# Performance work log

Hardware: AMD Instinct MI355X
Metric: run time of the kernel (lower is better)

## Reference

```python
import jax, jax.numpy as jnp
import numpy as np

B, S, D = 4, 2048, 1024

def _xavier(key, shape):
    bound = float(np.sqrt(6.0 / (shape[0] + shape[1])))
    return jax.random.uniform(key, shape, dtype=jnp.float32, minval=-bound, maxval=bound)

def setup_inputs() -> dict:
    key = jax.random.key(0)
    k0, k1, k2, k3 = jax.random.split(key, 4)
    return {
        "embeddings": jax.random.normal(k0, (B, S, D), dtype=jnp.float32),
        "W_Q": _xavier(k1, (D, D)),
        "W_K": _xavier(k2, (D, D)),
        "W_V": _xavier(k3, (D, D)),
    }

def reference(embeddings, W_Q, W_K, W_V):
    _, seq_len, d = embeddings.shape
    Q = embeddings @ W_Q                      # [B,S,D]
    K = embeddings @ W_K
    V = embeddings @ W_V
    scale = 1.0 / jnp.sqrt(jnp.float32(d))
    scores = jnp.einsum('bqd,bkd->bqk', Q, K) * scale   # [B,S,S]
    causal = jnp.tril(jnp.ones((seq_len, seq_len), dtype=bool))
    scores = jnp.where(causal[None, :, :], scores, -jnp.inf)
    probs = jax.nn.softmax(scores, axis=-1)
    return jnp.einsum('bqk,bkd->bqd', probs, V)
```

## Files before the change

kernel.cpp:

```cpp
#include <hip/hip_runtime.h>
#include <hip/hip_bf16.h>

#define BSZ 4
#define SEQ 2048
#define DIM 1024

typedef __attribute__((ext_vector_type(8))) short bf16x8;
typedef __attribute__((ext_vector_type(4))) float floatx4;

__device__ __forceinline__ unsigned short f2bf(float x) {
  union { float f; unsigned int u; } v; v.f = x;
  unsigned int r = v.u + 0x7fffu + ((v.u >> 16) & 1u);
  return (unsigned short)(r >> 16);
}

template <typename T> __device__ __forceinline__ void store_c(T* p, float v);
template <> __device__ __forceinline__ void store_c<float>(float* p, float v) { *p = v; }
template <> __device__ __forceinline__ void store_c<unsigned short>(unsigned short* p, float v) { *p = f2bf(v); }

__global__ __launch_bounds__(256) void prep(const float* __restrict__ E,
                                            const float* __restrict__ Wq,
                                            const float* __restrict__ Wk,
                                            const float* __restrict__ Wv,
                                            unsigned short* __restrict__ Ebf,
                                            unsigned short* __restrict__ Wqbf,
                                            unsigned short* __restrict__ Wkbf,
                                            unsigned short* __restrict__ WtV,
                                            float* __restrict__ rsum) {
  __shared__ float tile[32][33];
  int b = blockIdx.x;
  int tid = threadIdx.x;
  if (b < 10240) {
    const float* src;
    unsigned short* dst;
    int base;
    if (b < 8192) {
      if (b < 8) {
        int j = b * 1024 + tid * 4;
        *(float4*)(rsum + j) = make_float4(0.f, 0.f, 0.f, 0.f);
      }
      src = E; dst = Ebf; base = b;
    } else if (b < 9216) {
      src = Wq; dst = Wqbf; base = b - 8192;
    } else {
      src = Wk; dst = Wkbf; base = b - 9216;
    }
    int i = (base * 256 + tid) * 4;
    float4 v = *(const float4*)(src + i);
    ushort4 o;
    o.x = f2bf(v.x); o.y = f2bf(v.y); o.z = f2bf(v.z); o.w = f2bf(v.w);
    *(ushort4*)(dst + i) = o;
  } else {
    int rb = b - 10240;
    int bx = rb & 31, by = rb >> 5;
    int n0 = bx * 32, k0 = by * 32;
    int tx = tid & 31, ty = tid >> 5;
    for (int r = ty; r < 32; r += 8)
      tile[r][tx] = Wv[(size_t)(k0 + r) * DIM + n0 + tx];
    __syncthreads();
    for (int r = ty; r < 32; r += 8)
      WtV[(size_t)(n0 + r) * DIM + k0 + tx] = f2bf(tile[tx][r]);
  }
}

__device__ __forceinline__ void gload16(const unsigned short* g, unsigned short* l) {
  __builtin_amdgcn_global_load_lds(
      (const __attribute__((address_space(1))) unsigned int*)g,
      (__attribute__((address_space(3))) unsigned int*)l, 16, 0, 0);
}

#define NT_PROJ 32

template <int BMt>
__device__ __forceinline__ void proj_core(
    const unsigned short* __restrict__ A,
    const unsigned short* __restrict__ Bm,
    unsigned short* __restrict__ C, int ldc, int m0, int n0,
    unsigned short* sAr, unsigned short* sBr) {
  constexpr int LPA = BMt / 128;
  constexpr int LPT = LPA + 2;
  constexpr int FR  = BMt / 32;
  constexpr int TA  = BMt * 32;
  constexpr int TB  = 256 * 32;

  const int tid = threadIdx.x;
  const int lane = tid & 63;
  const int wid = tid >> 6;
  const int wm = (wid >> 2) * (BMt / 2);
  const int wn = (wid & 3) * 64;
  const int lr = lane & 15, lq = lane >> 4;

  const int srow = tid >> 2;
  const int schunk = (tid & 3) ^ ((tid >> 3) & 3);
  const unsigned short* gA = A + (size_t)(m0 + srow) * DIM + schunk * 8;
  const unsigned short* gB = Bm + (size_t)(n0 + srow) * DIM + schunk * 8;
  unsigned short* lA = sAr + 16 * 32 * wid;
  unsigned short* lB = sBr + 16 * 32 * wid;
  const size_t swG = (size_t)128 * DIM;

#define STAGE_A(T) do { int rb_ = (T) & 3; \
    gload16(gA + (size_t)(T) * 32, lA + rb_ * TA); \
    if constexpr (LPA == 2) gload16(gA + (size_t)(T) * 32 + swG, lA + rb_ * TA + 4096); } while (0)
#define STAGE_B(T) do { int rb_ = (T) & 3; \
    gload16(gB + (size_t)(T) * 32,       lB + rb_ * TB); \
    gload16(gB + (size_t)(T) * 32 + swG, lB + rb_ * TB + 4096); } while (0)
#define ARD(rb_, rowv) (*(const bf16x8*)&sAr[(rb_) * TA + (rowv) * 32 + (lq ^ (((rowv) >> 1) & 3)) * 8])
#define BRD(rb_, rowv) (*(const bf16x8*)&sBr[(rb_) * TB + (rowv) * 32 + (lq ^ (((rowv) >> 1) & 3)) * 8])

  floatx4 acc[FR][4] = {};

  STAGE_A(0); STAGE_B(0);
  STAGE_A(1); STAGE_B(1);
  STAGE_A(2); STAGE_B(2);
  if constexpr (LPT == 4) asm volatile("s_waitcnt vmcnt(8)" ::: "memory");
  else                    asm volatile("s_waitcnt vmcnt(6)" ::: "memory");
  __builtin_amdgcn_s_barrier();

#pragma unroll 4
  for (int T = 0; T < NT_PROJ; ++T) {
    const int rb = T & 3;
    bf16x8 af[4], bfr[4];
#pragma unroll
    for (int j = 0; j < 4; ++j) bfr[j] = BRD(rb, wn + j * 16 + lr);
#pragma unroll
    for (int i = 0; i < 4; ++i) af[i] = ARD(rb, wm + i * 16 + lr);
    if (T + 3 < NT_PROJ) {
      STAGE_A(T + 3);
      if constexpr (BMt == 128) STAGE_B(T + 3);
    }
    __builtin_amdgcn_s_barrier();
    __builtin_amdgcn_s_setprio(1);
#pragma unroll
    for (int i = 0; i < 4; ++i)
#pragma unroll
      for (int j = 0; j < 4; ++j)
        acc[i][j] = __builtin_amdgcn_mfma_f32_16x16x32_bf16(af[i], bfr[j], acc[i][j], 0, 0, 0);
    __builtin_amdgcn_s_setprio(0);
    if constexpr (BMt == 256) {
      __builtin_amdgcn_s_barrier();
#pragma unroll
      for (int i = 0; i < 4; ++i) af[i] = ARD(rb, wm + 64 + i * 16 + lr);
      if (T + 3 < NT_PROJ) STAGE_B(T + 3);
      __builtin_amdgcn_s_barrier();
      __builtin_amdgcn_s_setprio(1);
#pragma unroll
      for (int i = 0; i < 4; ++i)
#pragma unroll
        for (int j = 0; j < 4; ++j)
          acc[4 + i][j] = __builtin_amdgcn_mfma_f32_16x16x32_bf16(af[i], bfr[j], acc[4 + i][j], 0, 0, 0);
      __builtin_amdgcn_s_setprio(0);
    }
    if (T < NT_PROJ - 3) {
      if constexpr (LPT == 4) asm volatile("s_waitcnt vmcnt(8)" ::: "memory");
      else                    asm volatile("s_waitcnt vmcnt(6)" ::: "memory");
    } else if (T == NT_PROJ - 3) {
      if constexpr (LPT == 4) asm volatile("s_waitcnt vmcnt(4)" ::: "memory");
      else                    asm volatile("s_waitcnt vmcnt(3)" ::: "memory");
    } else if (T == NT_PROJ - 2) {
      asm volatile("s_waitcnt vmcnt(0)" ::: "memory");
    }
    __builtin_amdgcn_s_barrier();
  }
#undef STAGE_A
#undef STAGE_B
#undef ARD
#undef BRD

#pragma unroll
  for (int i = 0; i < FR; ++i) {
    int rbase = m0 + wm + i * 16 + lq * 4;
#pragma unroll
    for (int j = 0; j < 4; ++j) {
      int col = n0 + wn + j * 16 + lr;
#pragma unroll
      for (int r = 0; r < 4; ++r)
        C[(size_t)(rbase + r) * ldc + col] = f2bf(acc[i][j][r]);
    }
  }
}

__global__ __launch_bounds__(512, 2) void bulk1(
    const unsigned short* __restrict__ Wkbf,
    const unsigned short* __restrict__ Wqbf,
    const unsigned short* __restrict__ Ebf,
    const unsigned short* __restrict__ WtV,
    unsigned short* __restrict__ Mt,
    unsigned short* __restrict__ Vt) {
  __shared__ __align__(16) unsigned short sA[16384];
  __shared__ __align__(16) unsigned short sB[32768];
  int x = blockIdx.x;
  if (x < 32) {
    proj_core<128>(Wkbf, Wqbf, Mt, DIM, (x >> 2) * 128, (x & 3) * 256, sA, sB);
  } else {
    x -= 32;
    proj_core<128>(WtV, Ebf, Vt, BSZ * SEQ, (x >> 5) * 128, (x & 31) * 256, sA, sB);
  }
}

__global__ __launch_bounds__(512, 2) void bulk2(
    const unsigned short* __restrict__ Ebf,
    const unsigned short* __restrict__ Mt,
    unsigned short* __restrict__ EM) {
  __shared__ __align__(16) unsigned short sA[16384];
  __shared__ __align__(16) unsigned short sB[32768];
  int x = blockIdx.x;
  proj_core<128>(Ebf, Mt, EM, DIM, (x >> 2) * 128, (x & 3) * 256, sA, sB);
}

template <typename OutT, int MODE>
__global__ __launch_bounds__(256, 2) void gemm_ring(
    const unsigned short* __restrict__ A, int lda, long long strideA,
    const unsigned short* __restrict__ B, int ldb, long long strideB,
    OutT* __restrict__ C, int ldc, long long strideC,
    int Kdim, float scale, float* __restrict__ rowsum) {
  int m0, n0;
  if constexpr (MODE == 1) {
    int t = blockIdx.x;
    int mt = 0;
    while (((mt + 1) * (mt + 2)) / 2 <= t) mt++;
    int nt = t - (mt * (mt + 1)) / 2;
    m0 = mt * 128; n0 = nt * 128;
  } else {
    int yy = ((blockIdx.z >> 1) & 1) ? blockIdx.y : (gridDim.y - 1 - blockIdx.y);
    m0 = yy * 128;
    n0 = blockIdx.x * 128;
  }
  const int Keff = (MODE == 2) ? min(Kdim, m0 + 128) : Kdim;
  const int NT = Keff >> 5;
  A += (long long)blockIdx.z * strideA;
  B += (long long)blockIdx.z * strideB;
  C += (long long)blockIdx.z * strideC;
  rowsum += (size_t)blockIdx.z * SEQ;

  __shared__ __align__(16) unsigned short sA[4 * 4096];
  __shared__ __align__(16) unsigned short sB[4 * 4096];

  const int tid = threadIdx.x;
  const int lane = tid & 63;
  const int wid = tid >> 6;
  const int wm = (wid >> 1) * 64, wn = (wid & 1) * 64;
  const int lr = lane & 15, lq = lane >> 4;

  const int schunk = (tid & 3) ^ ((tid >> 3) & 3);
  const unsigned short* gA = A + (size_t)(m0 + (tid >> 2)) * lda + schunk * 8;
  const unsigned short* gB = B + (size_t)(n0 + (tid >> 2)) * ldb + schunk * 8;
  unsigned short* lA = sA + wid * 512;
  unsigned short* lB = sB + wid * 512;
  const size_t sGA = (size_t)64 * lda, sGB = (size_t)64 * ldb;

#define RSTAGE(T) do { int rb_ = (T) & 3; \
    gload16(gA + (size_t)(T) * 32,       lA + rb_ * 4096); \
    gload16(gA + (size_t)(T) * 32 + sGA, lA + rb_ * 4096 + 2048); \
    gload16(gB + (size_t)(T) * 32,       lB + rb_ * 4096); \
    gload16(gB + (size_t)(T) * 32 + sGB, lB + rb_ * 4096 + 2048); } while (0)
#define RARD(rb_, rowv) (*(const bf16x8*)&sA[(rb_) * 4096 + (rowv) * 32 + (lq ^ (((rowv) >> 1) & 3)) * 8])
#define RBRD(rb_, rowv) (*(const bf16x8*)&sB[(rb_) * 4096 + (rowv) * 32 + (lq ^ (((rowv) >> 1) & 3)) * 8])

  floatx4 acc[4][4] = {};

  RSTAGE(0); RSTAGE(1); RSTAGE(2);
  asm volatile("s_waitcnt vmcnt(8)" ::: "memory");
  __builtin_amdgcn_s_barrier();

  for (int T = 0; T < NT; ++T) {
    const int rb = T & 3;
    bf16x8 af[4], bfr[4];
#pragma unroll
    for (int j = 0; j < 4; ++j) bfr[j] = RBRD(rb, wn + j * 16 + lr);
#pragma unroll
    for (int i = 0; i < 4; ++i) af[i] = RARD(rb, wm + i * 16 + lr);
    if (T + 3 < NT) RSTAGE(T + 3);
    __builtin_amdgcn_s_barrier();
    __builtin_amdgcn_s_setprio(1);
#pragma unroll
    for (int i = 0; i < 4; ++i)
#pragma unroll
      for (int j = 0; j < 4; ++j)
        acc[i][j] = __builtin_amdgcn_mfma_f32_16x16x32_bf16(af[i], bfr[j], acc[i][j], 0, 0, 0);
    __builtin_amdgcn_s_setprio(0);
    if (T < NT - 3)       asm volatile("s_waitcnt vmcnt(8)" ::: "memory");
    else if (T == NT - 3) asm volatile("s_waitcnt vmcnt(4)" ::: "memory");
    else if (T == NT - 2) asm volatile("s_waitcnt vmcnt(0)" ::: "memory");
    __builtin_amdgcn_s_barrier();
  }
#undef RSTAGE
#undef RARD
#undef RBRD

  if constexpr (MODE == 1) {
#pragma unroll
    for (int i = 0; i < 4; i++) {
      int rbase = m0 + wm + i * 16 + lq * 4;
      float s0 = 0.f, s1 = 0.f, s2 = 0.f, s3 = 0.f;
#pragma unroll
      for (int j = 0; j < 4; j++) {
        int col = n0 + wn + j * 16 + lr;
        float e0 = (col <= rbase + 0) ? __expf(acc[i][j][0] * scale) : 0.0f;
        float e1 = (col <= rbase + 1) ? __expf(acc[i][j][1] * scale) : 0.0f;
        float e2 = (col <= rbase + 2) ? __expf(acc[i][j][2] * scale) : 0.0f;
        float e3 = (col <= rbase + 3) ? __expf(acc[i][j][3] * scale) : 0.0f;
        store_c(&C[(size_t)(rbase + 0) * ldc + col], e0);
        store_c(&C[(size_t)(rbase + 1) * ldc + col], e1);
        store_c(&C[(size_t)(rbase + 2) * ldc + col], e2);
        store_c(&C[(size_t)(rbase + 3) * ldc + col], e3);
        s0 += e0; s1 += e1; s2 += e2; s3 += e3;
      }
#pragma unroll
      for (int m = 1; m < 16; m <<= 1) {
        s0 += __shfl_xor(s0, m, 64);
        s1 += __shfl_xor(s1, m, 64);
        s2 += __shfl_xor(s2, m, 64);
        s3 += __shfl_xor(s3, m, 64);
      }
      if (lr == 0) {
        atomicAdd(&rowsum[rbase + 0], s0);
        atomicAdd(&rowsum[rbase + 1], s1);
        atomicAdd(&rowsum[rbase + 2], s2);
        atomicAdd(&rowsum[rbase + 3], s3);
      }
    }
  } else {
#pragma unroll
    for (int i = 0; i < 4; i++) {
      int rbase = m0 + wm + i * 16 + lq * 4;
      float i0 = 1.0f / rowsum[rbase + 0];
      float i1 = 1.0f / rowsum[rbase + 1];
      float i2 = 1.0f / rowsum[rbase + 2];
      float i3 = 1.0f / rowsum[rbase + 3];
#pragma unroll
      for (int j = 0; j < 4; j++) {
        int col = n0 + wn + j * 16 + lr;
        store_c(&C[(size_t)(rbase + 0) * ldc + col], acc[i][j][0] * i0);
        store_c(&C[(size_t)(rbase + 1) * ldc + col], acc[i][j][1] * i1);
        store_c(&C[(size_t)(rbase + 2) * ldc + col], acc[i][j][2] * i2);
        store_c(&C[(size_t)(rbase + 3) * ldc + col], acc[i][j][3] * i3);
      }
    }
  }
}

extern "C" void kernel_launch(void* const* d_in, const int* in_sizes, int n_in,
                              void* d_out, int out_size, void* d_ws, size_t ws_size,
                              hipStream_t stream) {
  const float* E  = (const float*)d_in[0];
  const float* Wq = (const float*)d_in[1];
  const float* Wk = (const float*)d_in[2];
  const float* Wv = (const float*)d_in[3];
  float* out = (float*)d_out;

  char* ws = (char*)d_ws;
  size_t off = 0;
  auto alloc = [&](size_t bytes) {
    void* p = ws + off;
    off += (bytes + 255) & ~(size_t)255;
    return p;
  };
  const size_t M_ALL = (size_t)BSZ * SEQ;
  unsigned short* Ebf  = (unsigned short*)alloc(M_ALL * DIM * 2);
  unsigned short* Wqbf = (unsigned short*)alloc((size_t)DIM * DIM * 2);
  unsigned short* Wkbf = (unsigned short*)alloc((size_t)DIM * DIM * 2);
  unsigned short* WtV  = (unsigned short*)alloc((size_t)DIM * DIM * 2);
  unsigned short* Mt   = (unsigned short*)alloc((size_t)DIM * DIM * 2);
  unsigned short* EM   = (unsigned short*)alloc(M_ALL * DIM * 2);
  unsigned short* Vt   = (unsigned short*)alloc((size_t)DIM * M_ALL * 2);
  unsigned short* ExpS = (unsigned short*)alloc((size_t)BSZ * SEQ * SEQ * 2);
  float*          Rsum = (float*)alloc((size_t)BSZ * SEQ * 4);

  prep<<<dim3(11264), dim3(256), 0, stream>>>(E, Wq, Wk, Wv, Ebf, Wqbf, Wkbf, WtV, Rsum);

  bulk1<<<dim3(288), dim3(512), 0, stream>>>(Wkbf, Wqbf, Ebf, WtV, Mt, Vt);

  bulk2<<<dim3(256), dim3(512), 0, stream>>>(Ebf, Mt, EM);

  gemm_ring<unsigned short, 1><<<dim3(136, 1, BSZ), dim3(256), 0, stream>>>(
      EM, DIM, (long long)SEQ * DIM,
      Ebf, DIM, (long long)SEQ * DIM,
      ExpS, SEQ, (long long)SEQ * SEQ,
      DIM, 0.03125f , Rsum);

  gemm_ring<float, 2><<<dim3(8, 16, BSZ), dim3(256), 0, stream>>>(
      ExpS, SEQ, (long long)SEQ * SEQ,
      Vt, (int)M_ALL, (long long)SEQ,
      out, DIM, (long long)SEQ * DIM,
      SEQ, 1.0f, Rsum);
}
```

Baseline: 241.0 us.

## Compute Wk·Wqᵀ inside prep from fp32 and merge projection kernels

The small Mt = Wk·Wqᵀ GEMM moves into the prep kernel as 64 extra blocks. These blocks load fp32 weights directly, convert them to bf16 in registers and use a register-prefetched LDS MFMA loop. This drops the separate bf16 copies of Wq and Wk and their buffers. With Mt ready after prep, the V projection and the E·Mt projection merge into one launch, removing a kernel boundary and a dependent stage. The cost is that 64 heavy GEMM blocks now run inside a memory-bound conversion kernel and may form a tail.

```diff
diff --git a/kernel.cpp b/kernel.cpp
--- a/kernel.cpp
+++ b/kernel.cpp
@@ -12,6 +12,17 @@
   union { float f; unsigned int u; } v; v.f = x;
   unsigned int r = v.u + 0x7fffu + ((v.u >> 16) & 1u);
   return (unsigned short)(r >> 16);
+}
+
+__device__ __forceinline__ uint4 ld8f(const float* p) {
+  float4 a = *(const float4*)p;
+  float4 b = *(const float4*)(p + 4);
+  uint4 u;
+  u.x = (unsigned)f2bf(a.x) | ((unsigned)f2bf(a.y) << 16);
+  u.y = (unsigned)f2bf(a.z) | ((unsigned)f2bf(a.w) << 16);
+  u.z = (unsigned)f2bf(b.x) | ((unsigned)f2bf(b.y) << 16);
+  u.w = (unsigned)f2bf(b.z) | ((unsigned)f2bf(b.w) << 16);
+  return u;
 }
 
 template <typename T> __device__ __forceinline__ void store_c(T* p, float v);
@@ -23,43 +34,109 @@
                                             const float* __restrict__ Wk,
                                             const float* __restrict__ Wv,
                                             unsigned short* __restrict__ Ebf,
-                                            unsigned short* __restrict__ Wqbf,
-                                            unsigned short* __restrict__ Wkbf,
                                             unsigned short* __restrict__ WtV,
+                                            unsigned short* __restrict__ Mt,
                                             float* __restrict__ rsum) {
-  __shared__ float tile[32][33];
+  __shared__ __align__(16) unsigned short As[128][72];
+  __shared__ __align__(16) unsigned short Bs[128][72];
   int b = blockIdx.x;
   int tid = threadIdx.x;
-  if (b < 10240) {
-    const float* src;
-    unsigned short* dst;
-    int base;
-    if (b < 8192) {
-      if (b < 8) {
-        int j = b * 1024 + tid * 4;
-        *(float4*)(rsum + j) = make_float4(0.f, 0.f, 0.f, 0.f);
-      }
-      src = E; dst = Ebf; base = b;
-    } else if (b < 9216) {
-      src = Wq; dst = Wqbf; base = b - 8192;
-    } else {
-      src = Wk; dst = Wkbf; base = b - 9216;
+
+  if (b < 64) {
+    int m0 = (b >> 3) * 128, n0 = (b & 7) * 128;
+    int lane = tid & 63;
+    int wid = tid >> 6;
+    int wm = (wid >> 1) * 64, wn = (wid & 1) * 64;
+    int lr = lane & 15, lq = lane >> 4;
+    int row = tid >> 3;
+    int kc = (tid & 7) * 8;
+
+    const float* Ab = Wk + (size_t)(m0 + row) * DIM + kc;
+    const float* Bb = Wq + (size_t)(n0 + row) * DIM + kc;
+    size_t la = (size_t)32 * DIM;
+
+    uint4 ra0 = ld8f(Ab);
+    uint4 ra1 = ld8f(Ab + la);
+    uint4 ra2 = ld8f(Ab + 2 * la);
+    uint4 ra3 = ld8f(Ab + 3 * la);
+    uint4 rb0 = ld8f(Bb);
+    uint4 rb1 = ld8f(Bb + la);
+    uint4 rb2 = ld8f(Bb + 2 * la);
+    uint4 rb3 = ld8f(Bb + 3 * la);
+
+    floatx4 acc[4][4] = {};
+
+    for (int k0 = 0; k0 < DIM; k0 += 64) {
+      __syncthreads();
+      *(uint4*)&As[row][kc]      = ra0;
+      *(uint4*)&As[row + 32][kc] = ra1;
+      *(uint4*)&As[row + 64][kc] = ra2;
+      *(uint4*)&As[row + 96][kc] = ra3;
+      *(uint4*)&Bs[row][kc]      = rb0;
+      *(uint4*)&Bs[row + 32][kc] = rb1;
+      *(uint4*)&Bs[row + 64][kc] = rb2;
+      *(uint4*)&Bs[row + 96][kc] = rb3;
+      if (k0 + 64 < DIM) {
+        const float* An = Ab + k0 + 64;
+        const float* Bn = Bb + k0 + 64;
+        ra0 = ld8f(An);
+        ra1 = ld8f(An + la);
+        ra2 = ld8f(An + 2 * la);
+        ra3 = ld8f(An + 3 * la);
+        rb0 = ld8f(Bn);
+        rb1 = ld8f(Bn + la);
+        rb2 = ld8f(Bn + 2 * la);
+        rb3 = ld8f(Bn + 3 * la);
+      }
+      __syncthreads();
+#pragma unroll
+      for (int kk = 0; kk < 64; kk += 32) {
+        bf16x8 af[4], bfr[4];
+        int kl = kk + lq * 8;
+#pragma unroll
+        for (int i = 0; i < 4; i++) af[i] = *(const bf16x8*)&As[wm + i * 16 + lr][kl];
+#pragma unroll
+        for (int j = 0; j < 4; j++) bfr[j] = *(const bf16x8*)&Bs[wn + j * 16 + lr][kl];
+#pragma unroll
+        for (int i = 0; i < 4; i++)
+#pragma unroll
+          for (int j = 0; j < 4; j++)
+            acc[i][j] = __builtin_amdgcn_mfma_f32_16x16x32_bf16(af[i], bfr[j], acc[i][j], 0, 0, 0);
+      }
+    }
+#pragma unroll
+    for (int i = 0; i < 4; i++) {
+      int rbase = m0 + wm + i * 16 + lq * 4;
+#pragma unroll
+      for (int j = 0; j < 4; j++) {
+        int col = n0 + wn + j * 16 + lr;
+#pragma unroll
+        for (int r = 0; r < 4; r++)
+          Mt[(size_t)(rbase + r) * DIM + col] = f2bf(acc[i][j][r]);
+      }
+    }
+  } else if (b < 8256) {
+    int base = b - 64;
+    if (base < 8) {
+      int j = base * 1024 + tid * 4;
+      *(float4*)(rsum + j) = make_float4(0.f, 0.f, 0.f, 0.f);
     }
     int i = (base * 256 + tid) * 4;
-    float4 v = *(const float4*)(src + i);
+    float4 v = *(const float4*)(E + i);
     ushort4 o;
     o.x = f2bf(v.x); o.y = f2bf(v.y); o.z = f2bf(v.z); o.w = f2bf(v.w);
-    *(ushort4*)(dst + i) = o;
+    *(ushort4*)(Ebf + i) = o;
   } else {
-    int rb = b - 10240;
+    float* tileF = (float*)As;
+    int rb = b - 8256;
     int bx = rb & 31, by = rb >> 5;
     int n0 = bx * 32, k0 = by * 32;
     int tx = tid & 31, ty = tid >> 5;
     for (int r = ty; r < 32; r += 8)
-      tile[r][tx] = Wv[(size_t)(k0 + r) * DIM + n0 + tx];
+      tileF[r * 33 + tx] = Wv[(size_t)(k0 + r) * DIM + n0 + tx];
     __syncthreads();
     for (int r = ty; r < 32; r += 8)
-      WtV[(size_t)(n0 + r) * DIM + k0 + tx] = f2bf(tile[tx][r]);
+      WtV[(size_t)(n0 + r) * DIM + k0 + tx] = f2bf(tileF[tx * 33 + r]);
   }
 }
 
@@ -179,32 +256,21 @@
   }
 }
 
-__global__ __launch_bounds__(512, 2) void bulk1(
-    const unsigned short* __restrict__ Wkbf,
-    const unsigned short* __restrict__ Wqbf,
+__global__ __launch_bounds__(512, 2) void bulk(
     const unsigned short* __restrict__ Ebf,
     const unsigned short* __restrict__ WtV,
-    unsigned short* __restrict__ Mt,
-    unsigned short* __restrict__ Vt) {
-  __shared__ __align__(16) unsigned short sA[16384];
-  __shared__ __align__(16) unsigned short sB[32768];
-  int x = blockIdx.x;
-  if (x < 32) {
-    proj_core<128>(Wkbf, Wqbf, Mt, DIM, (x >> 2) * 128, (x & 3) * 256, sA, sB);
-  } else {
-    x -= 32;
-    proj_core<128>(WtV, Ebf, Vt, BSZ * SEQ, (x >> 5) * 128, (x & 31) * 256, sA, sB);
-  }
-}
-
-__global__ __launch_bounds__(512, 2) void bulk2(
-    const unsigned short* __restrict__ Ebf,
     const unsigned short* __restrict__ Mt,
+    unsigned short* __restrict__ Vt,
     unsigned short* __restrict__ EM) {
   __shared__ __align__(16) unsigned short sA[16384];
   __shared__ __align__(16) unsigned short sB[32768];
   int x = blockIdx.x;
-  proj_core<128>(Ebf, Mt, EM, DIM, (x >> 2) * 128, (x & 3) * 256, sA, sB);
+  if (x < 256) {
+    proj_core<128>(WtV, Ebf, Vt, BSZ * SEQ, (x >> 5) * 128, (x & 31) * 256, sA, sB);
+  } else {
+    x -= 256;
+    proj_core<128>(Ebf, Mt, EM, DIM, (x >> 2) * 128, (x & 3) * 256, sA, sB);
+  }
 }
 
 template <typename OutT, int MODE>
@@ -357,8 +423,6 @@
   };
   const size_t M_ALL = (size_t)BSZ * SEQ;
   unsigned short* Ebf  = (unsigned short*)alloc(M_ALL * DIM * 2);
-  unsigned short* Wqbf = (unsigned short*)alloc((size_t)DIM * DIM * 2);
-  unsigned short* Wkbf = (unsigned short*)alloc((size_t)DIM * DIM * 2);
   unsigned short* WtV  = (unsigned short*)alloc((size_t)DIM * DIM * 2);
   unsigned short* Mt   = (unsigned short*)alloc((size_t)DIM * DIM * 2);
   unsigned short* EM   = (unsigned short*)alloc(M_ALL * DIM * 2);
@@ -366,11 +430,9 @@
   unsigned short* ExpS = (unsigned short*)alloc((size_t)BSZ * SEQ * SEQ * 2);
   float*          Rsum = (float*)alloc((size_t)BSZ * SEQ * 4);
 
-  prep<<<dim3(11264), dim3(256), 0, stream>>>(E, Wq, Wk, Wv, Ebf, Wqbf, Wkbf, WtV, Rsum);
-
-  bulk1<<<dim3(288), dim3(512), 0, stream>>>(Wkbf, Wqbf, Ebf, WtV, Mt, Vt);
-
-  bulk2<<<dim3(256), dim3(512), 0, stream>>>(Ebf, Mt, EM);
+  prep<<<dim3(9280), dim3(256), 0, stream>>>(E, Wq, Wk, Wv, Ebf, WtV, Mt, Rsum);
+
+  bulk<<<dim3(512), dim3(512), 0, stream>>>(Ebf, WtV, Mt, Vt, EM);
 
   gemm_ring<unsigned short, 1><<<dim3(136, 1, BSZ), dim3(256), 0, stream>>>(
       EM, DIM, (long long)SEQ * DIM,
```

Result: no change. 244.2 us (+1.3%).
